# Optimization experiments

Measured on AMD Instinct MI355X. Metric: run time of the kernel, lower is better.

The kernel has to match this reference:

```python
import jax, jax.numpy as jnp
import numpy as np

N, S, D, H, NF, E = 65536, 24, 64, 4, 256, 1048576
Hd = D // H
EPS = 1e-5


def _pe_table(nf, d):
    pe = np.zeros((nf, d), np.float32)
    pos = np.arange(nf, dtype=np.float32)[:, None]
    div = np.exp(np.arange(0, d, 2, dtype=np.float32) * -(np.log(10000.0) / d))
    pe[:, 0::2] = np.sin(pos * div)
    pe[:, 1::2] = np.cos(pos * div)
    return jnp.asarray(pe)


def setup_inputs() -> dict:
    key = jax.random.key(0)
    ks = iter(jax.random.split(key, 64))
    g = lambda shape: jax.random.normal(next(ks), shape, jnp.float32) * 0.02
    z = lambda shape: jnp.zeros(shape, jnp.float32)
    o = lambda shape: jnp.ones(shape, jnp.float32)
    inp = {
        'x': jax.random.normal(next(ks), (N, S), jnp.float32),
        'edge_index': jax.random.randint(next(ks), (2, E), 0, N, jnp.int32),
        'Wi': g((S, D)), 'bi': z((D,)), 'pe': _pe_table(NF, D),
        # per-head TransformerConv params (H separate convs, heads=1 each)
        'Wq': g((H, D, Hd)), 'Wk': g((H, D, Hd)), 'Wv': g((H, D, Hd)),
        'bq': z((H, Hd)), 'bk': z((H, Hd)), 'bv': z((H, Hd)),
        'Ws': g((H, D, Hd)), 'bs': z((H, Hd)),
        'Wo': g((D, D)), 'bo': z((D,)), 'gln_g': o((D,)), 'gln_b': z((D,)),
        # temporal MHA + FFN
        'Wqt': g((D, D)), 'Wkt': g((D, D)), 'Wvt': g((D, D)),
        'bqt': z((D,)), 'bkt': z((D,)), 'bvt': z((D,)),
        'Wot': g((D, D)), 'bot': z((D,)),
        'ln1_g': o((D,)), 'ln1_b': z((D,)),
        'W1': g((D, 2 * D)), 'b1': z((2 * D,)), 'W2': g((2 * D, D)), 'b2': z((D,)),
        'ln2_g': o((D,)), 'ln2_b': z((D,)),
        # aggregation + prediction head
        'Wa1': g((NF * D, D)), 'ba1': z((D,)), 'Wa2': g((D, D // 2)), 'ba2': z((D // 2,)),
        'Wh1': g((D // 2, D // 4)), 'bh1': z((D // 4,)), 'Wh2': g((D // 4, 1)), 'bh2': z((1,)),
    }
    return inp


def _ln(x, g, b):
    m = jnp.mean(x, axis=-1, keepdims=True)
    v = jnp.var(x, axis=-1, keepdims=True)
    return (x - m) * jax.lax.rsqrt(v + EPS) * g + b


def reference(x, edge_index, Wi, bi, pe, Wq, Wk, Wv, bq, bk, bv, Ws, bs, Wo, bo,
              gln_g, gln_b, Wqt, Wkt, Wvt, bqt, bkt, bvt, Wot, bot, ln1_g, ln1_b,
              W1, b1, W2, b2, ln2_g, ln2_b, Wa1, ba1, Wa2, ba2, Wh1, bh1, Wh2, bh2):
    n, nf, d = x.shape[0], pe.shape[0], pe.shape[1]
    bsz = n // nf
    scale = 1.0 / np.sqrt(Hd).astype(np.float32)

    # input projection + positional encoding (repeated per graph)
    h = x @ Wi + bi + jnp.tile(pe, (bsz, 1))  # [N, D]

    # ---- multi-head TransformerConv graph attention (gather-softmax-scatter) ----
    src, dst = edge_index[0], edge_index[1]
    q = jnp.einsum('nd,hdk->nhk', h, Wq) + bq  # [N,H,Hd]
    k = jnp.einsum('nd,hdk->nhk', h, Wk) + bk
    v = jnp.einsum('nd,hdk->nhk', h, Wv) + bv
    logits = jnp.sum(q[dst] * k[src], axis=-1) * scale  # [E,H]
    m = jax.ops.segment_max(logits, dst, num_segments=N)  # [N,H]
    ex = jnp.exp(logits - m[dst])
    denom = jax.ops.segment_sum(ex, dst, num_segments=N)  # [N,H]
    alpha = ex / denom[dst]
    agg = jax.ops.segment_sum(alpha[:, :, None] * v[src], dst, num_segments=N)  # [N,H,Hd]
    skip = jnp.einsum('nd,hdk->nhk', h, Ws) + bs  # root weight (lin_skip)
    out = (agg + skip).reshape(n, d) @ Wo + bo
    h = _ln(out + h, gln_g, gln_b)  # residual (in_dim == out_dim)

    # ---- temporal transformer over the NF node axis ----
    xt = h.reshape(bsz, nf, d)
    qt = (xt @ Wqt + bqt).reshape(bsz, nf, H, Hd)
    kt = (xt @ Wkt + bkt).reshape(bsz, nf, H, Hd)
    vt = (xt @ Wvt + bvt).reshape(bsz, nf, H, Hd)
    sc = jnp.einsum('bihd,bjhd->bhij', qt, kt) * scale
    a = jax.nn.softmax(sc, axis=-1)
    attn = jnp.einsum('bhij,bjhd->bihd', a, vt).reshape(bsz, nf, d)
    attn = attn @ Wot + bot
    xt = _ln(xt + attn, ln1_g, ln1_b)
    ff = jax.nn.relu(xt @ W1 + b1) @ W2 + b2
    xt = _ln(xt + ff, ln2_g, ln2_b)

    # ---- aggregation + prediction head ----
    xf = xt.reshape(bsz, nf * d)
    a1 = jax.nn.relu(xf @ Wa1 + ba1)
    a2 = jax.nn.relu(a1 @ Wa2 + ba2)
    h1 = jax.nn.relu(a2 @ Wh1 + bh1)
    out = jax.nn.sigmoid(h1 @ Wh2 + bh2)
    return out.squeeze(-1)  # [B]
```

## Files before the change

kernel.cpp:

```cpp
#include <hip/hip_runtime.h>
#include <hip/hip_fp16.h>
#include <math.h>

#define NN 65536
#define SIN 24
#define DD 64
#define HH 4
#define HDIM 16
#define NFRM 256
#define NE 1048576
#define BSZ 256
#define EPSLN 1e-5f
#define SCL 0.25f
#define AKS 32
#define WTN 55296

typedef __attribute__((ext_vector_type(8))) short bf16x8;
typedef __attribute__((ext_vector_type(4))) float f32x4;

__device__ __forceinline__ unsigned short f2bf(float f) {
  unsigned u = __float_as_uint(f);
  return (unsigned short)((u + 0x7FFFu + ((u >> 16) & 1u)) >> 16);
}
__device__ __forceinline__ float bf2f(unsigned short b) {
  return __uint_as_float(((unsigned)b) << 16);
}
__device__ __forceinline__ float bflo(unsigned u) {
  return __uint_as_float(u << 16);
}
__device__ __forceinline__ float bfhi(unsigned u) {
  return __uint_as_float(u & 0xFFFF0000u);
}
__device__ __forceinline__ unsigned f2e5(float f) {
  unsigned short h = __half_as_ushort(__float2half(f));
  unsigned r = (unsigned)h + 0x7Fu + ((h >> 8) & 1u);
  return (r >> 8) & 0xFFu;
}
__device__ __forceinline__ float h2fb(unsigned short b) {
  return __half2float(__ushort_as_half(b));
}
#define KLO(u) h2fb((unsigned short)((u) & 0xFF00u))
#define KHI(u) h2fb((unsigned short)(((u) >> 16) & 0xFF00u))
#define VLO(u) h2fb((unsigned short)(((u) << 8) & 0xFF00u))
#define VHI(u) h2fb((unsigned short)(((u) >> 8) & 0xFF00u))

__device__ __forceinline__ void stage_bf(const unsigned short* __restrict__ src,
                                         unsigned short* dst, int n8, int DK, int ST, int tid) {
  int dk8 = DK >> 3;
  for (int idx = tid; idx < n8; idx += 256) {
    int row = idx / dk8, c = (idx % dk8) * 8;
    *(uint4*)(dst + row * ST + c) = *(const uint4*)(src + (size_t)row * DK + c);
  }
}

__global__ void k_wprep(const float* __restrict__ Wo, const float* __restrict__ Wot,
                        const float* __restrict__ Wqt, const float* __restrict__ Wkt,
                        const float* __restrict__ Wvt, const float* __restrict__ W1,
                        const float* __restrict__ W2, const float* __restrict__ Wq,
                        const float* __restrict__ Wk, const float* __restrict__ Wv,
                        const float* __restrict__ Wsk, const float* __restrict__ Wi,
                        unsigned short* __restrict__ wt) {
  int i = blockIdx.x * 256 + threadIdx.x;
  if (i >= WTN) return;
  float v;
  if (i < 4096)       { int t = i;         int j = t >> 6, d = t & 63; v = Wo[d * 64 + j]; }
  else if (i < 8192)  { int t = i - 4096;  int j = t >> 6, d = t & 63; v = Wot[d * 64 + j]; }
  else if (i < 12288) { int t = i - 8192;  int j = t >> 6, d = t & 63; v = Wqt[d * 64 + j]; }
  else if (i < 16384) { int t = i - 12288; int j = t >> 6, d = t & 63; v = Wkt[d * 64 + j]; }
  else if (i < 20480) { int t = i - 16384; int j = t >> 6, d = t & 63; v = Wvt[d * 64 + j]; }
  else if (i < 28672) { int t = i - 20480; int j = t >> 6, d = t & 63; v = W1[d * 128 + j]; }
  else if (i < 36864) { int t = i - 28672; int j = t >> 7, d = t & 127; v = W2[d * 64 + j]; }
  else if (i < 40960) { int t = i - 36864; int j = t >> 6, d = t & 63; v = Wq[(j >> 4) * 1024 + d * 16 + (j & 15)]; }
  else if (i < 45056) { int t = i - 40960; int j = t >> 6, d = t & 63; v = Wk[(j >> 4) * 1024 + d * 16 + (j & 15)]; }
  else if (i < 49152) { int t = i - 45056; int j = t >> 6, d = t & 63; v = Wv[(j >> 4) * 1024 + d * 16 + (j & 15)]; }
  else if (i < 53248) { int t = i - 49152; int j = t >> 6, d = t & 63; v = Wsk[(j >> 4) * 1024 + d * 16 + (j & 15)]; }
  else                { int t = i - 53248; int j = t >> 5, k = t & 31; v = (k < SIN) ? Wi[k * 64 + j] : 0.f; }
  wt[i] = f2bf(v);
}

__global__ void k_wprep2(const float* __restrict__ Wa1, unsigned short* __restrict__ wa1t) {
  __shared__ float tile[64][65];
  int kb = blockIdx.x;
  int t = threadIdx.x;
  int c = t & 63, r0 = t >> 6;
  int k0 = kb * 64;
#pragma unroll
  for (int i = 0; i < 16; ++i) {
    int r = r0 + i * 4;
    tile[r][c] = Wa1[(size_t)(k0 + r) * 64 + c];
  }
  __syncthreads();
#pragma unroll
  for (int i = 0; i < 16; ++i) {
    int o = r0 + i * 4;
    wa1t[(size_t)o * 16384 + k0 + c] = f2bf(tile[c][o]);
  }
}

__global__ void __launch_bounds__(256)
k_qkvs_m(const float* __restrict__ x, const unsigned short* __restrict__ wt,
         const float* __restrict__ bi, const float* __restrict__ pe,
         const float* __restrict__ bq, const float* __restrict__ bk,
         const float* __restrict__ bv, const float* __restrict__ bs,
         unsigned short* __restrict__ us_h, unsigned short* __restrict__ us_q,
         unsigned short* __restrict__ kv8, unsigned short* __restrict__ us_sk) {
  __shared__ unsigned short Xs[64 * 72];
  __shared__ unsigned short Ws4[4 * 64 * 72];
  unsigned short* Xi  = Ws4;
  unsigned short* WiS = Ws4 + 64 * 40;
  int tid = threadIdx.x;
  int n0 = blockIdx.x * 64;
  for (int idx = tid; idx < 2048; idx += 256) {
    int row = idx >> 5, k = idx & 31;
    Xi[row * 40 + k] = (k < SIN) ? f2bf(x[(size_t)(n0 + row) * SIN + k]) : 0;
    WiS[row * 40 + k] = wt[53248 + row * 32 + k];
  }
  __syncthreads();
  int lane = tid & 63, w = tid >> 6;
  int c = lane & 15, g = lane >> 4;
  int rowb = n0 + w * 16 + 4 * g;
  f32x4 hb[4];
  {
    bf16x8 xf = *(const bf16x8*)(Xi + (w * 16 + c) * 40 + g * 8);
#pragma unroll
    for (int jj = 0; jj < 4; ++jj)
      hb[jj] = __builtin_amdgcn_mfma_f32_16x16x32_bf16(xf,
                 *(const bf16x8*)(WiS + (jj * 16 + c) * 40 + g * 8),
                 (f32x4){0.f, 0.f, 0.f, 0.f}, 0, 0, 0);
  }
#pragma unroll
  for (int jj = 0; jj < 4; ++jj) {
    int col = jj * 16 + c;
    float bb = bi[col];
#pragma unroll
    for (int r = 0; r < 4; ++r) {
      int row = w * 16 + 4 * g + r;
      float hv = hb[jj][r] + bb + pe[((n0 + row) & (NFRM - 1)) * DD + col];
      unsigned short hbf = f2bf(hv);
      us_h[(size_t)(n0 + row) * DD + col] = hbf;
      Xs[row * 72 + col] = hbf;
    }
  }
  __syncthreads();
  stage_bf(wt + 36864, Ws4, 64 * 8, 64, 72, tid);
  stage_bf(wt + 40960, Ws4 + 4608, 64 * 8, 64, 72, tid);
  stage_bf(wt + 45056, Ws4 + 9216, 64 * 8, 64, 72, tid);
  stage_bf(wt + 49152, Ws4 + 13824, 64 * 8, 64, 72, tid);
  __syncthreads();
  f32x4 aq[4], ak[4], av[4], as_[4];
#pragma unroll
  for (int jj = 0; jj < 4; ++jj) {
#pragma unroll
    for (int r = 0; r < 4; ++r) { aq[jj][r] = 0.f; ak[jj][r] = 0.f; av[jj][r] = 0.f; as_[jj][r] = 0.f; }
  }
  const unsigned short* xrow = Xs + (w * 16 + c) * 72 + g * 8;
#pragma unroll
  for (int kk = 0; kk < 2; ++kk) {
    bf16x8 af = *(const bf16x8*)(xrow + kk * 32);
#pragma unroll
    for (int jj = 0; jj < 4; ++jj) {
      int boff = (jj * 16 + c) * 72 + kk * 32 + g * 8;
      aq[jj] = __builtin_amdgcn_mfma_f32_16x16x32_bf16(af, *(const bf16x8*)(Ws4 + boff), aq[jj], 0, 0, 0);
      ak[jj] = __builtin_amdgcn_mfma_f32_16x16x32_bf16(af, *(const bf16x8*)(Ws4 + 4608 + boff), ak[jj], 0, 0, 0);
      av[jj] = __builtin_amdgcn_mfma_f32_16x16x32_bf16(af, *(const bf16x8*)(Ws4 + 9216 + boff), av[jj], 0, 0, 0);
      as_[jj] = __builtin_amdgcn_mfma_f32_16x16x32_bf16(af, *(const bf16x8*)(Ws4 + 13824 + boff), as_[jj], 0, 0, 0);
    }
  }
#pragma unroll
  for (int jj = 0; jj < 4; ++jj) {
    int col = jj * 16 + c;
    float bqj = bq[col], bkj = bk[col], bvj = bv[col], bsj = bs[col];
#pragma unroll
    for (int r = 0; r < 4; ++r) {
      size_t o = (size_t)(rowb + r) * 64 + col;
      us_q[o] = f2bf(aq[jj][r] + bqj);
      kv8[o] = (unsigned short)((f2e5(ak[jj][r] + bkj) << 8) | f2e5(av[jj][r] + bvj));
      us_sk[o] = f2bf(as_[jj][r] + bsj);
    }
  }
}

__global__ void k_hist(const int* __restrict__ ei, int* __restrict__ hist) {
  __shared__ int h2[2][256];
  int t = threadIdx.x;
  h2[0][t] = 0; h2[1][t] = 0;
  __syncthreads();
  int sub = (t >> 6) & 1;
  int base = blockIdx.x * 4096;
#pragma unroll
  for (int r = 0; r < 16; ++r)
    atomicAdd(&h2[sub][ei[NE + base + r * 256 + t] >> 8], 1);
  __syncthreads();
  hist[t * 256 + blockIdx.x] = h2[0][t] + h2[1][t];
}

__global__ void k_hscan(int* __restrict__ hist, int* __restrict__ btot) {
  __shared__ int s[256];
  int t = threadIdx.x, bkt = blockIdx.x;
  int v = hist[bkt * 256 + t];
  s[t] = v; __syncthreads();
  for (int off = 1; off < 256; off <<= 1) {
    int x = (t >= off) ? s[t - off] : 0;
    __syncthreads();
    s[t] += x;
    __syncthreads();
  }
  hist[bkt * 256 + t] = s[t] - v;
  if (t == 255) btot[bkt] = s[255];
}

__global__ void k_bscan(const int* __restrict__ btot, int* __restrict__ bbase) {
  __shared__ int s[256];
  int t = threadIdx.x;
  int v = btot[t];
  s[t] = v; __syncthreads();
  for (int off = 1; off < 256; off <<= 1) {
    int x = (t >= off) ? s[t - off] : 0;
    __syncthreads();
    s[t] += x;
    __syncthreads();
  }
  bbase[t] = s[t] - v;
}

__global__ void k_passB(const int* __restrict__ ei, const int* __restrict__ hist,
                        const int* __restrict__ bbase, int* __restrict__ pairs) {
  __shared__ int cur[256];
  int t = threadIdx.x;
  cur[t] = bbase[t] + hist[t * 256 + blockIdx.x];
  __syncthreads();
  int base = blockIdx.x * 4096;
#pragma unroll
  for (int r = 0; r < 16; ++r) {
    int e = base + r * 256 + t;
    int src = ei[e], dst = ei[NE + e];
    int pos = atomicAdd(&cur[dst >> 8], 1);
    pairs[pos] = ((dst & 255) << 16) | src;
  }
}

__global__ void k_passC(const int* __restrict__ pairs, const int* __restrict__ bbase,
                        const int* __restrict__ btot, int* __restrict__ rowptr,
                        int* __restrict__ srcs) {
  __shared__ int cnt[256];
  __shared__ int s[256];
  int t = threadIdx.x, bkt = blockIdx.x;
  cnt[t] = 0;
  __syncthreads();
  int base = bbase[bkt], n = btot[bkt];
  int pr[18];
#pragma unroll
  for (int j = 0; j < 18; ++j) {
    int i = t + j * 256;
    if (i >= n) break;
    int p = pairs[base + i];
    pr[j] = p;
    atomicAdd(&cnt[p >> 16], 1);
  }
  for (int i = t + 18 * 256; i < n; i += 256)
    atomicAdd(&cnt[pairs[base + i] >> 16], 1);
  __syncthreads();
  int v = cnt[t];
  s[t] = v; __syncthreads();
  for (int off = 1; off < 256; off <<= 1) {
    int x = (t >= off) ? s[t - off] : 0;
    __syncthreads();
    s[t] += x;
    __syncthreads();
  }
  int rp = base + s[t] - v;
  rowptr[bkt * 256 + t] = rp;
  if (bkt == 0 && t == 0) rowptr[NN] = NE;
  __syncthreads();
  cnt[t] = rp;
  __syncthreads();
#pragma unroll
  for (int j = 0; j < 18; ++j) {
    int i = t + j * 256;
    if (i >= n) break;
    int p = pr[j];
    int pos = atomicAdd(&cnt[p >> 16], 1);
    srcs[pos] = p & 0xFFFF;
  }
  for (int i = t + 18 * 256; i < n; i += 256) {
    int p = pairs[base + i];
    int pos = atomicAdd(&cnt[p >> 16], 1);
    srcs[pos] = p & 0xFFFF;
  }
}

__global__ void __launch_bounds__(256)
k_gattn(const unsigned short* __restrict__ us_q, const unsigned short* __restrict__ kv8,
        const int* __restrict__ rowptr, const int* __restrict__ srcs,
        const unsigned short* __restrict__ us_sk, unsigned short* __restrict__ tmpb) {
  __shared__ float red[8][32][17];
  int tid = threadIdx.x;
  int lane = tid & 63;
  int slot = (tid >> 5) & 7;
  int e = (lane >> 2) & 7, h = lane & 3;
  int dst = (blockIdx.x << 3) + slot;
  float qv[16];
  {
    const uint4* qp = (const uint4*)(us_q + (size_t)dst * 64 + h * 16);
    uint4 q0 = qp[0], q1 = qp[1];
    qv[0] = bflo(q0.x); qv[1] = bfhi(q0.x); qv[2] = bflo(q0.y); qv[3] = bfhi(q0.y);
    qv[4] = bflo(q0.z); qv[5] = bfhi(q0.z); qv[6] = bflo(q0.w); qv[7] = bfhi(q0.w);
    qv[8] = bflo(q1.x); qv[9] = bfhi(q1.x); qv[10] = bflo(q1.y); qv[11] = bfhi(q1.y);
    qv[12] = bflo(q1.z); qv[13] = bfhi(q1.z); qv[14] = bflo(q1.w); qv[15] = bfhi(q1.w);
  }
  int beg = rowptr[dst], end = rowptr[dst + 1];
  float l = 0.f;
  float acc[16];
#pragma unroll
  for (int i = 0; i < 16; ++i) acc[i] = 0.f;

  int idx = beg + e;
  int src = (idx < end) ? srcs[idx] : 0;
  const uint4* kp = (const uint4*)(kv8 + (size_t)src * 64 + h * 16);
  uint4 A = kp[0], Bv = kp[1];
  for (;;) {
    int nidx = idx + 8;
    bool any_next = __any(nidx < end);
    uint4 nA, nB;
    if (any_next) {
      int nsrc = (nidx < end) ? srcs[nidx] : 0;
      const uint4* np = (const uint4*)(kv8 + (size_t)nsrc * 64 + h * 16);
      nA = np[0]; nB = np[1];
    }
    bool valid = idx < end;
    float s;
    s  = KLO(A.x) * qv[0]   + KHI(A.x) * qv[1]   + KLO(A.y) * qv[2]   + KHI(A.y) * qv[3];
    s += KLO(A.z) * qv[4]   + KHI(A.z) * qv[5]   + KLO(A.w) * qv[6]   + KHI(A.w) * qv[7];
    s += KLO(Bv.x) * qv[8]  + KHI(Bv.x) * qv[9]  + KLO(Bv.y) * qv[10] + KHI(Bv.y) * qv[11];
    s += KLO(Bv.z) * qv[12] + KHI(Bv.z) * qv[13] + KLO(Bv.w) * qv[14] + KHI(Bv.w) * qv[15];
    float pex = valid ? __expf(s * SCL) : 0.f;
    l += pex;
    acc[0]  += pex * VLO(A.x);  acc[1]  += pex * VHI(A.x);
    acc[2]  += pex * VLO(A.y);  acc[3]  += pex * VHI(A.y);
    acc[4]  += pex * VLO(A.z);  acc[5]  += pex * VHI(A.z);
    acc[6]  += pex * VLO(A.w);  acc[7]  += pex * VHI(A.w);
    acc[8]  += pex * VLO(Bv.x); acc[9]  += pex * VHI(Bv.x);
    acc[10] += pex * VLO(Bv.y); acc[11] += pex * VHI(Bv.y);
    acc[12] += pex * VLO(Bv.z); acc[13] += pex * VHI(Bv.z);
    acc[14] += pex * VLO(Bv.w); acc[15] += pex * VHI(Bv.w);
    if (!any_next) break;
    A = nA; Bv = nB;
    idx = nidx;
  }
  l += __shfl_xor(l, 4); l += __shfl_xor(l, 8); l += __shfl_xor(l, 16);
  float* rw = &red[slot][lane & 31][0];
#pragma unroll
  for (int i = 0; i < 16; ++i) rw[i] = acc[i];
  int r32 = lane & 31;
  int h0 = r32 >> 4, i0 = r32 & 15;
  float l0 = __shfl(l, (lane & 32) + h0);
  float l1 = __shfl(l, (lane & 32) + h0 + 2);
  float s0 = 0.f, s1 = 0.f;
#pragma unroll
  for (int ep = 0; ep < 8; ++ep) {
    s0 += red[slot][ep * 4 + h0][i0];
    s1 += red[slot][ep * 4 + h0 + 2][i0];
  }
  bool nonempty = end > beg;
  float a0 = nonempty ? s0 / l0 : 0.f;
  float a1 = nonempty ? s1 / l1 : 0.f;
  size_t o0 = (size_t)dst * 64 + r32;
  tmpb[o0] = f2bf(a0 + bf2f(us_sk[o0]));
  tmpb[o0 + 32] = f2bf(a1 + bf2f(us_sk[o0 + 32]));
}

__global__ void __launch_bounds__(256)
k_mlqkvt(const unsigned short* __restrict__ in1, const unsigned short* __restrict__ wt,
         const float* __restrict__ bias, const float* __restrict__ gam,
         const float* __restrict__ bet, unsigned short* __restrict__ us_h,
         const float* __restrict__ bqt, const float* __restrict__ bkt,
         const float* __restrict__ bvt,
         unsigned short* __restrict__ qt, unsigned short* __restrict__ kt,
         unsigned short* __restrict__ vt) {
  __shared__ unsigned short A[64 * 72];
  __shared__ unsigned short B[3 * 64 * 72];
  int tid = threadIdx.x;
  int n0 = blockIdx.x * 64;
  stage_bf(in1 + (size_t)n0 * 64, A, 64 * 8, 64, 72, tid);
  stage_bf(wt + 0, B, 64 * 8, 64, 72, tid);
  __syncthreads();
  int lane = tid & 63, w = tid >> 6;
  int c = lane & 15, g = lane >> 4;
  f32x4 acc[4];
#pragma unroll
  for (int j = 0; j < 4; ++j) { acc[j][0] = 0.f; acc[j][1] = 0.f; acc[j][2] = 0.f; acc[j][3] = 0.f; }
  const unsigned short* xrow = A + (w * 16 + c) * 72 + g * 8;
#pragma unroll
  for (int kk = 0; kk < 2; ++kk) {
    bf16x8 af = *(const bf16x8*)(xrow + kk * 32);
#pragma unroll
    for (int j = 0; j < 4; ++j)
      acc[j] = __builtin_amdgcn_mfma_f32_16x16x32_bf16(af,
                 *(const bf16x8*)(B + (j * 16 + c) * 72 + kk * 32 + g * 8), acc[j], 0, 0, 0);
  }
  int rowb = n0 + w * 16 + 4 * g;
  float o[4][4];
#pragma unroll
  for (int j = 0; j < 4; ++j) {
    int col = j * 16 + c;
    float bb = bias[col];
#pragma unroll
    for (int r = 0; r < 4; ++r)
      o[j][r] = acc[j][r] + bb + bf2f(us_h[(size_t)(rowb + r) * 64 + col]);
  }
#pragma unroll
  for (int r = 0; r < 4; ++r) {
    float s = (o[0][r] + o[1][r]) + (o[2][r] + o[3][r]);
    float s2 = (o[0][r] * o[0][r] + o[1][r] * o[1][r]) + (o[2][r] * o[2][r] + o[3][r] * o[3][r]);
#pragma unroll
    for (int off = 1; off <= 8; off <<= 1) {
      s += __shfl_xor(s, off);
      s2 += __shfl_xor(s2, off);
    }
    float mean = s * (1.0f / 64.0f);
    float var = s2 * (1.0f / 64.0f) - mean * mean;
    float rs = rsqrtf(var + EPSLN);
#pragma unroll
    for (int j = 0; j < 4; ++j)
      o[j][r] = (o[j][r] - mean) * rs * gam[j * 16 + c] + bet[j * 16 + c];
  }
  __syncthreads();
#pragma unroll
  for (int j = 0; j < 4; ++j) {
    int col = j * 16 + c;
#pragma unroll
    for (int r = 0; r < 4; ++r) {
      unsigned short ob = f2bf(o[j][r]);
      us_h[(size_t)(rowb + r) * 64 + col] = ob;
      A[(w * 16 + 4 * g + r) * 72 + col] = ob;
    }
  }
  stage_bf(wt + 8192, B, 64 * 8, 64, 72, tid);
  stage_bf(wt + 12288, B + 4608, 64 * 8, 64, 72, tid);
  stage_bf(wt + 16384, B + 9216, 64 * 8, 64, 72, tid);
  __syncthreads();
  f32x4 aq[4], ak[4], av[4];
#pragma unroll
  for (int j = 0; j < 4; ++j) {
#pragma unroll
    for (int r = 0; r < 4; ++r) { aq[j][r] = 0.f; ak[j][r] = 0.f; av[j][r] = 0.f; }
  }
#pragma unroll
  for (int kk = 0; kk < 2; ++kk) {
    bf16x8 af = *(const bf16x8*)(xrow + kk * 32);
#pragma unroll
    for (int j = 0; j < 4; ++j) {
      int boff = (j * 16 + c) * 72 + kk * 32 + g * 8;
      aq[j] = __builtin_amdgcn_mfma_f32_16x16x32_bf16(af, *(const bf16x8*)(B + boff), aq[j], 0, 0, 0);
      ak[j] = __builtin_amdgcn_mfma_f32_16x16x32_bf16(af, *(const bf16x8*)(B + 4608 + boff), ak[j], 0, 0, 0);
      av[j] = __builtin_amdgcn_mfma_f32_16x16x32_bf16(af, *(const bf16x8*)(B + 9216 + boff), av[j], 0, 0, 0);
    }
  }
#pragma unroll
  for (int j = 0; j < 4; ++j) {
    int col = j * 16 + c;
    float bqj = bqt[col], bkj = bkt[col], bvj = bvt[col];
#pragma unroll
    for (int r = 0; r < 4; ++r) {
      size_t oo = (size_t)j * (NN * 16) + (size_t)(rowb + r) * 16 + c;
      qt[oo] = f2bf(aq[j][r] + bqj);
      kt[oo] = f2bf(ak[j][r] + bkj);
      vt[oo] = f2bf(av[j][r] + bvj);
    }
  }
}

#define PST 40
#define VTS 264
__global__ void __launch_bounds__(256)
k_tattn(const unsigned short* __restrict__ qtb, const unsigned short* __restrict__ ktb,
        const unsigned short* __restrict__ vtb, unsigned short* __restrict__ attnb) {
  int b = blockIdx.x >> 2, hh = blockIdx.x & 3;
  __shared__ unsigned short Qs[NFRM][16];
  __shared__ unsigned short Ks[NFRM][16];
  __shared__ unsigned short Vt[16][VTS];
  __shared__ unsigned short Ps[4][16][PST];
  int t = threadIdx.x;
  int wv = t >> 6, lane = t & 63;
  int g = lane >> 4, c = lane & 15;
  {
    size_t src = (size_t)hh * (NN * 16) + ((size_t)b * NFRM + t) * 16;
    const uint4* qsrc = (const uint4*)(qtb + src);
    const uint4* ksrc = (const uint4*)(ktb + src);
    const uint4* vsrc = (const uint4*)(vtb + src);
    ((uint4*)Qs[t])[0] = qsrc[0]; ((uint4*)Qs[t])[1] = qsrc[1];
    ((uint4*)Ks[t])[0] = ksrc[0]; ((uint4*)Ks[t])[1] = ksrc[1];
    uint4 v0 = vsrc[0], v1 = vsrc[1];
    unsigned vv[8] = {v0.x, v0.y, v0.z, v0.w, v1.x, v1.y, v1.z, v1.w};
#pragma unroll
    for (int d = 0; d < 8; ++d) {
      Vt[2 * d][t] = (unsigned short)(vv[d] & 0xFFFFu);
      Vt[2 * d + 1][t] = (unsigned short)(vv[d] >> 16);
    }
  }
  __syncthreads();
  const bf16x8 zf = {0, 0, 0, 0, 0, 0, 0, 0};
  unsigned short (*P)[PST] = Ps[wv];
  for (int qt0 = wv; qt0 < 16; qt0 += 4) {
    bf16x8 qf = zf;
    if (g < 2) qf = *(const bf16x8*)&Qs[qt0 * 16 + c][g * 8];
    f32x4 O = {0.f, 0.f, 0.f, 0.f};
    float lacc[4] = {0.f, 0.f, 0.f, 0.f};
    for (int jp = 0; jp < 8; ++jp) {
#pragma unroll
      for (int half = 0; half < 2; ++half) {
        int jt = jp * 2 + half;
        bf16x8 kf = zf;
        if (g < 2) kf = *(const bf16x8*)&Ks[jt * 16 + c][g * 8];
        f32x4 S = __builtin_amdgcn_mfma_f32_16x16x32_bf16(qf, kf,
                    (f32x4){0.f, 0.f, 0.f, 0.f}, 0, 0, 0);
#pragma unroll
        for (int r = 0; r < 4; ++r) {
          float p = __expf(S[r] * SCL);
          lacc[r] += p;
          P[4 * g + r][half * 16 + c] = f2bf(p);
        }
      }
      bf16x8 pf = *(const bf16x8*)&P[c][g * 8];
      bf16x8 vf = *(const bf16x8*)&Vt[c][jp * 32 + g * 8];
      O = __builtin_amdgcn_mfma_f32_16x16x32_bf16(pf, vf, O, 0, 0, 0);
    }
#pragma unroll
    for (int r = 0; r < 4; ++r) {
      float s = lacc[r];
      s += __shfl_xor(s, 1); s += __shfl_xor(s, 2);
      s += __shfl_xor(s, 4); s += __shfl_xor(s, 8);
      lacc[r] = 1.0f / s;
    }
    size_t obase = ((size_t)b * NFRM + qt0 * 16) * DD + hh * 16;
#pragma unroll
    for (int r = 0; r < 4; ++r)
      attnb[obase + (size_t)(4 * g + r) * DD + c] = f2bf(O[r] * lacc[r]);
  }
}

__global__ void __launch_bounds__(256)
k_blk2(const unsigned short* __restrict__ attn, const unsigned short* __restrict__ wt,
       const unsigned short* __restrict__ res, const float* __restrict__ bot,
       const float* __restrict__ l1g, const float* __restrict__ l1b,
       const float* __restrict__ b1, const float* __restrict__ b2,
       const float* __restrict__ l2g, const float* __restrict__ l2b,
       unsigned short* __restrict__ xtb) {
  __shared__ unsigned short XLs[64 * 72];
  __shared__ unsigned short BufW[128 * 72];
  __shared__ unsigned short BufX[64 * 136];
  int tid = threadIdx.x;
  int n0 = blockIdx.x * 64;
  int lane = tid & 63, w = tid >> 6;
  int c = lane & 15, g = lane >> 4;
  int rowb = n0 + w * 16 + 4 * g;
  stage_bf(attn + (size_t)n0 * 64, BufX, 64 * 8, 64, 72, tid);
  stage_bf(wt + 4096, BufW, 64 * 8, 64, 72, tid);
  __syncthreads();
  f32x4 acc[4];
#pragma unroll
  for (int j = 0; j < 4; ++j) { acc[j][0] = 0.f; acc[j][1] = 0.f; acc[j][2] = 0.f; acc[j][3] = 0.f; }
  const unsigned short* xrow = BufX + (w * 16 + c) * 72 + g * 8;
#pragma unroll
  for (int kk = 0; kk < 2; ++kk) {
    bf16x8 af = *(const bf16x8*)(xrow + kk * 32);
#pragma unroll
    for (int j = 0; j < 4; ++j)
      acc[j] = __builtin_amdgcn_mfma_f32_16x16x32_bf16(af,
                 *(const bf16x8*)(BufW + (j * 16 + c) * 72 + kk * 32 + g * 8), acc[j], 0, 0, 0);
  }
  float x[4][4];
#pragma unroll
  for (int j = 0; j < 4; ++j) {
    int col = j * 16 + c;
    float bb = bot[col];
#pragma unroll
    for (int r = 0; r < 4; ++r)
      x[j][r] = acc[j][r] + bb + bf2f(res[(size_t)(rowb + r) * 64 + col]);
  }
#pragma unroll
  for (int r = 0; r < 4; ++r) {
    float s = (x[0][r] + x[1][r]) + (x[2][r] + x[3][r]);
    float s2 = (x[0][r] * x[0][r] + x[1][r] * x[1][r]) + (x[2][r] * x[2][r] + x[3][r] * x[3][r]);
#pragma unroll
    for (int off = 1; off <= 8; off <<= 1) {
      s += __shfl_xor(s, off);
      s2 += __shfl_xor(s2, off);
    }
    float mean = s * (1.0f / 64.0f);
    float var = s2 * (1.0f / 64.0f) - mean * mean;
    float rs = rsqrtf(var + EPSLN);
#pragma unroll
    for (int j = 0; j < 4; ++j)
      x[j][r] = (x[j][r] - mean) * rs * l1g[j * 16 + c] + l1b[j * 16 + c];
  }
  __syncthreads();
#pragma unroll
  for (int j = 0; j < 4; ++j)
#pragma unroll
    for (int r = 0; r < 4; ++r)
      XLs[(w * 16 + 4 * g + r) * 72 + j * 16 + c] = f2bf(x[j][r]);
  stage_bf(wt + 20480, BufW, 128 * 8, 64, 72, tid);
  __syncthreads();
  f32x4 ua[8];
#pragma unroll
  for (int j = 0; j < 8; ++j) { ua[j][0] = 0.f; ua[j][1] = 0.f; ua[j][2] = 0.f; ua[j][3] = 0.f; }
  const unsigned short* xrow2 = XLs + (w * 16 + c) * 72 + g * 8;
#pragma unroll
  for (int kk = 0; kk < 2; ++kk) {
    bf16x8 af = *(const bf16x8*)(xrow2 + kk * 32);
#pragma unroll
    for (int j = 0; j < 8; ++j)
      ua[j] = __builtin_amdgcn_mfma_f32_16x16x32_bf16(af,
                *(const bf16x8*)(BufW + (j * 16 + c) * 72 + kk * 32 + g * 8), ua[j], 0, 0, 0);
  }
#pragma unroll
  for (int j = 0; j < 8; ++j) {
    int col = j * 16 + c;
    float bb = b1[col];
#pragma unroll
    for (int r = 0; r < 4; ++r)
      BufX[(w * 16 + 4 * g + r) * 136 + col] = f2bf(fmaxf(ua[j][r] + bb, 0.f));
  }
  __syncthreads();
  stage_bf(wt + 28672, BufW, 64 * 16, 128, 136, tid);
  __syncthreads();
  f32x4 ya[4];
#pragma unroll
  for (int j = 0; j < 4; ++j) { ya[j][0] = 0.f; ya[j][1] = 0.f; ya[j][2] = 0.f; ya[j][3] = 0.f; }
  const unsigned short* urow = BufX + (w * 16 + c) * 136 + g * 8;
#pragma unroll
  for (int kk = 0; kk < 4; ++kk) {
    bf16x8 af = *(const bf16x8*)(urow + kk * 32);
#pragma unroll
    for (int j = 0; j < 4; ++j)
      ya[j] = __builtin_amdgcn_mfma_f32_16x16x32_bf16(af,
                *(const bf16x8*)(BufW + (j * 16 + c) * 136 + kk * 32 + g * 8), ya[j], 0, 0, 0);
  }
  float o2[4][4];
#pragma unroll
  for (int j = 0; j < 4; ++j) {
    int col = j * 16 + c;
    float bb = b2[col];
#pragma unroll
    for (int r = 0; r < 4; ++r)
      o2[j][r] = ya[j][r] + bb + x[j][r];
  }
#pragma unroll
  for (int r = 0; r < 4; ++r) {
    float s = (o2[0][r] + o2[1][r]) + (o2[2][r] + o2[3][r]);
    float s2 = (o2[0][r] * o2[0][r] + o2[1][r] * o2[1][r]) + (o2[2][r] * o2[2][r] + o2[3][r] * o2[3][r]);
#pragma unroll
    for (int off = 1; off <= 8; off <<= 1) {
      s += __shfl_xor(s, off);
      s2 += __shfl_xor(s2, off);
    }
    float mean = s * (1.0f / 64.0f);
    float var = s2 * (1.0f / 64.0f) - mean * mean;
    float rs = rsqrtf(var + EPSLN);
#pragma unroll
    for (int j = 0; j < 4; ++j)
      xtb[(size_t)(rowb + r) * 64 + j * 16 + c] =
          f2bf((o2[j][r] - mean) * rs * l2g[j * 16 + c] + l2b[j * 16 + c]);
  }
}

__global__ void __launch_bounds__(256)
k_agg1a_m(const unsigned short* __restrict__ xtb, const unsigned short* __restrict__ wa1t,
          float* __restrict__ part) {
  int ks = blockIdx.x >> 2, mt = blockIdx.x & 3;
  int t = threadIdx.x, lane = t & 63, w = t >> 6;
  int c = lane & 15, g = lane >> 4;
  int m0 = mt * 64;
  int k0 = ks * 512;
  f32x4 acc[4];
#pragma unroll
  for (int j = 0; j < 4; ++j) { acc[j][0] = 0.f; acc[j][1] = 0.f; acc[j][2] = 0.f; acc[j][3] = 0.f; }
  const unsigned short* arow = xtb + (size_t)(m0 + w * 16 + c) * 16384 + k0 + g * 8;
  const unsigned short* brow = wa1t + (size_t)c * 16384 + k0 + g * 8;
#pragma unroll 4
  for (int kk = 0; kk < 16; ++kk) {
    bf16x8 af = *(const bf16x8*)(arow + kk * 32);
#pragma unroll
    for (int j = 0; j < 4; ++j)
      acc[j] = __builtin_amdgcn_mfma_f32_16x16x32_bf16(af,
                 *(const bf16x8*)(brow + (size_t)j * 16 * 16384 + kk * 32), acc[j], 0, 0, 0);
  }
  int rowb = m0 + w * 16 + 4 * g;
#pragma unroll
  for (int j = 0; j < 4; ++j)
#pragma unroll
    for (int r = 0; r < 4; ++r)
      part[(size_t)ks * (BSZ * DD) + (size_t)(rowb + r) * 64 + j * 16 + c] = acc[j][r];
}

__global__ void k_head(const float* __restrict__ part, const float* __restrict__ ba1,
                       const float* __restrict__ Wa2, const float* __restrict__ ba2,
                       const float* __restrict__ Wh1, const float* __restrict__ bh1,
                       const float* __restrict__ Wh2, const float* __restrict__ bh2,
                       float* __restrict__ out) {
  int b = blockIdx.x, t = threadIdx.x;
  __shared__ float s1[64], s2[32], s3[16];
  float a0 = ba1[t];
#pragma unroll 8
  for (int ks = 0; ks < AKS; ++ks) a0 += part[(size_t)ks * (BSZ * DD) + b * 64 + t];
  s1[t] = fmaxf(a0, 0.f);
  __syncthreads();
  if (t < 32) {
    float a = ba2[t];
#pragma unroll 8
    for (int j = 0; j < 64; ++j) a += s1[j] * Wa2[j * 32 + t];
    s2[t] = fmaxf(a, 0.f);
  }
  __syncthreads();
  if (t < 16) {
    float a = bh1[t];
#pragma unroll
    for (int j = 0; j < 32; ++j) a += s2[j] * Wh1[j * 16 + t];
    s3[t] = fmaxf(a, 0.f);
  }
  __syncthreads();
  if (t == 0) {
    float a = bh2[0];
#pragma unroll
    for (int j = 0; j < 16; ++j) a += s3[j] * Wh2[j];
    out[b] = 1.0f / (1.0f + expf(-a));
  }
}

extern "C" void kernel_launch(void* const* d_in, const int* in_sizes, int n_in,
                              void* d_out, int out_size, void* d_ws, size_t ws_size,
                              hipStream_t stream) {
  const float* x   = (const float*)d_in[0];
  const int*   ei  = (const int*)d_in[1];
  const float* Wi  = (const float*)d_in[2];
  const float* bi  = (const float*)d_in[3];
  const float* pe  = (const float*)d_in[4];
  const float* Wq  = (const float*)d_in[5];
  const float* Wk  = (const float*)d_in[6];
  const float* Wv  = (const float*)d_in[7];
  const float* bq  = (const float*)d_in[8];
  const float* bk  = (const float*)d_in[9];
  const float* bv  = (const float*)d_in[10];
  const float* Ws  = (const float*)d_in[11];
  const float* bs  = (const float*)d_in[12];
  const float* Wo  = (const float*)d_in[13];
  const float* bo  = (const float*)d_in[14];
  const float* gg  = (const float*)d_in[15];
  const float* gb  = (const float*)d_in[16];
  const float* Wqt = (const float*)d_in[17];
  const float* Wkt = (const float*)d_in[18];
  const float* Wvt = (const float*)d_in[19];
  const float* bqt = (const float*)d_in[20];
  const float* bkt = (const float*)d_in[21];
  const float* bvt = (const float*)d_in[22];
  const float* Wot = (const float*)d_in[23];
  const float* bot = (const float*)d_in[24];
  const float* l1g = (const float*)d_in[25];
  const float* l1b = (const float*)d_in[26];
  const float* W1  = (const float*)d_in[27];
  const float* b1  = (const float*)d_in[28];
  const float* W2  = (const float*)d_in[29];
  const float* b2  = (const float*)d_in[30];
  const float* l2g = (const float*)d_in[31];
  const float* l2b = (const float*)d_in[32];
  const float* Wa1 = (const float*)d_in[33];
  const float* ba1 = (const float*)d_in[34];
  const float* Wa2 = (const float*)d_in[35];
  const float* ba2 = (const float*)d_in[36];
  const float* Wh1 = (const float*)d_in[37];
  const float* bh1 = (const float*)d_in[38];
  const float* Wh2 = (const float*)d_in[39];
  const float* bh2 = (const float*)d_in[40];
  float* out = (float*)d_out;

  const size_t ND = (size_t)NN * DD;

  unsigned short* us_h  = (unsigned short*)d_ws;
  unsigned short* us_q  = us_h + ND;
  unsigned short* kv8   = us_q + ND;
  unsigned short* us_sk = kv8 + ND;
  unsigned short* tmpb  = us_sk + ND;
  unsigned short* us_qt = tmpb + ND;
  unsigned short* us_kt = us_qt + ND;
  unsigned short* us_vt = us_kt + ND;
  unsigned short* attnb = us_vt + ND;
  unsigned short* xtb   = attnb + ND;
  float* f_part = (float*)(xtb + ND);
  int* i_srcs   = (int*)(f_part + (size_t)AKS * BSZ * DD);
  int* i_rowptr = i_srcs + NE;
  int* i_hist   = i_rowptr + NN + 4;
  int* i_btot   = i_hist + 65536;
  int* i_bbase  = i_btot + 256;
  int* i_pairs  = i_bbase + 256;
  unsigned short* wt = (unsigned short*)(i_pairs + NE);
  unsigned short* wa1t = wt + WTN;

  dim3 B(256);
  k_wprep<<<dim3((WTN + 255) / 256), B, 0, stream>>>(Wo, Wot, Wqt, Wkt, Wvt, W1, W2,
                                                     Wq, Wk, Wv, Ws, Wi, wt);
  k_wprep2<<<dim3(256), B, 0, stream>>>(Wa1, wa1t);
  k_qkvs_m<<<dim3(NN / 64), B, 0, stream>>>(x, wt, bi, pe, bq, bk, bv, bs,
                                            us_h, us_q, kv8, us_sk);
  k_hist <<<dim3(256), B, 0, stream>>>(ei, i_hist);
  k_hscan<<<dim3(256), B, 0, stream>>>(i_hist, i_btot);
  k_bscan<<<dim3(1),   B, 0, stream>>>(i_btot, i_bbase);
  k_passB<<<dim3(256), B, 0, stream>>>(ei, i_hist, i_bbase, i_pairs);
  k_passC<<<dim3(256), B, 0, stream>>>(i_pairs, i_bbase, i_btot, i_rowptr, i_srcs);
  k_gattn<<<dim3(NN / 8), B, 0, stream>>>(us_q, kv8, i_rowptr, i_srcs, us_sk, tmpb);
  k_mlqkvt<<<dim3(NN / 64), B, 0, stream>>>(tmpb, wt, bo, gg, gb, us_h,
                                            bqt, bkt, bvt, us_qt, us_kt, us_vt);
  k_tattn<<<dim3(BSZ * HH), B, 0, stream>>>(us_qt, us_kt, us_vt, attnb);
  k_blk2<<<dim3(NN / 64), B, 0, stream>>>(attnb, wt, us_h, bot, l1g, l1b, b1, b2,
                                          l2g, l2b, xtb);
  k_agg1a_m<<<dim3(AKS * 4), B, 0, stream>>>(xtb, wa1t, f_part);
  k_head<<<dim3(BSZ), dim3(64), 0, stream>>>(f_part, ba1, Wa2, ba2, Wh1, bh1, Wh2, bh2, out);
}
```

Before: 170.8 us.

## Fold bucket scan into passB/passC, use 16-bit source indices, prefetch srcs

Removes the single-block k_bscan launch by recomputing the 256-entry bucket prefix scan redundantly inside every block of passB and passC. Source indices are stored as unsigned short instead of int, halving the CSR srcs traffic. The graph-attention loop preloads the first three source indices up front to shorten the dependent index-then-gather chain. The cost is redundant scan work in each block and extra registers in k_gattn.

```diff
diff --git a/kernel.cpp b/kernel.cpp
--- a/kernel.cpp
+++ b/kernel.cpp
@@ -209,25 +209,20 @@
   if (t == 255) btot[bkt] = s[255];
 }
 
-__global__ void k_bscan(const int* __restrict__ btot, int* __restrict__ bbase) {
-  __shared__ int s[256];
+__global__ void k_passB(const int* __restrict__ ei, const int* __restrict__ hist,
+                        const int* __restrict__ btot, int* __restrict__ pairs) {
+  __shared__ int cur[256];
+  __shared__ int sc[256];
   int t = threadIdx.x;
   int v = btot[t];
-  s[t] = v; __syncthreads();
+  sc[t] = v; __syncthreads();
   for (int off = 1; off < 256; off <<= 1) {
-    int x = (t >= off) ? s[t - off] : 0;
+    int x = (t >= off) ? sc[t - off] : 0;
     __syncthreads();
-    s[t] += x;
+    sc[t] += x;
     __syncthreads();
   }
-  bbase[t] = s[t] - v;
-}
-
-__global__ void k_passB(const int* __restrict__ ei, const int* __restrict__ hist,
-                        const int* __restrict__ bbase, int* __restrict__ pairs) {
-  __shared__ int cur[256];
-  int t = threadIdx.x;
-  cur[t] = bbase[t] + hist[t * 256 + blockIdx.x];
+  cur[t] = (sc[t] - v) + hist[t * 256 + blockIdx.x];
   __syncthreads();
   int base = blockIdx.x * 4096;
 #pragma unroll
@@ -239,15 +234,26 @@
   }
 }
 
-__global__ void k_passC(const int* __restrict__ pairs, const int* __restrict__ bbase,
-                        const int* __restrict__ btot, int* __restrict__ rowptr,
-                        int* __restrict__ srcs) {
+__global__ void k_passC(const int* __restrict__ pairs, const int* __restrict__ btot,
+                        int* __restrict__ rowptr, unsigned short* __restrict__ srcs) {
   __shared__ int cnt[256];
   __shared__ int s[256];
+  __shared__ int eb[256];
   int t = threadIdx.x, bkt = blockIdx.x;
+  {
+    int v0 = btot[t];
+    s[t] = v0; __syncthreads();
+    for (int off = 1; off < 256; off <<= 1) {
+      int x = (t >= off) ? s[t - off] : 0;
+      __syncthreads();
+      s[t] += x;
+      __syncthreads();
+    }
+    eb[t] = s[t] - v0;
+  }
   cnt[t] = 0;
   __syncthreads();
-  int base = bbase[bkt], n = btot[bkt];
+  int base = eb[bkt], n = btot[bkt];
   int pr[18];
 #pragma unroll
   for (int j = 0; j < 18; ++j) {
@@ -280,18 +286,18 @@
     if (i >= n) break;
     int p = pr[j];
     int pos = atomicAdd(&cnt[p >> 16], 1);
-    srcs[pos] = p & 0xFFFF;
+    srcs[pos] = (unsigned short)(p & 0xFFFF);
   }
   for (int i = t + 18 * 256; i < n; i += 256) {
     int p = pairs[base + i];
     int pos = atomicAdd(&cnt[p >> 16], 1);
-    srcs[pos] = p & 0xFFFF;
+    srcs[pos] = (unsigned short)(p & 0xFFFF);
   }
 }
 
 __global__ void __launch_bounds__(256)
 k_gattn(const unsigned short* __restrict__ us_q, const unsigned short* __restrict__ kv8,
-        const int* __restrict__ rowptr, const int* __restrict__ srcs,
+        const int* __restrict__ rowptr, const unsigned short* __restrict__ srcs,
         const unsigned short* __restrict__ us_sk, unsigned short* __restrict__ tmpb) {
   __shared__ float red[8][32][17];
   int tid = threadIdx.x;
@@ -315,15 +321,20 @@
   for (int i = 0; i < 16; ++i) acc[i] = 0.f;
 
   int idx = beg + e;
-  int src = (idx < end) ? srcs[idx] : 0;
-  const uint4* kp = (const uint4*)(kv8 + (size_t)src * 64 + h * 16);
+  int src0 = (idx < end) ? (int)srcs[idx] : 0;
+  int psrc1 = (idx + 8 < end) ? (int)srcs[idx + 8] : 0;
+  int psrc2 = (idx + 16 < end) ? (int)srcs[idx + 16] : 0;
+  const uint4* kp = (const uint4*)(kv8 + (size_t)src0 * 64 + h * 16);
   uint4 A = kp[0], Bv = kp[1];
+  int batch = 0;
   for (;;) {
     int nidx = idx + 8;
     bool any_next = __any(nidx < end);
     uint4 nA, nB;
     if (any_next) {
-      int nsrc = (nidx < end) ? srcs[nidx] : 0;
+      int nsrc = (batch == 0) ? psrc1
+               : (batch == 1) ? psrc2
+               : ((nidx < end) ? (int)srcs[nidx] : 0);
       const uint4* np = (const uint4*)(kv8 + (size_t)nsrc * 64 + h * 16);
       nA = np[0]; nB = np[1];
     }
@@ -346,6 +357,7 @@
     if (!any_next) break;
     A = nA; Bv = nB;
     idx = nidx;
+    ++batch;
   }
   l += __shfl_xor(l, 4); l += __shfl_xor(l, 8); l += __shfl_xor(l, 16);
   float* rw = &red[slot][lane & 31][0];
@@ -787,12 +799,11 @@
   unsigned short* attnb = us_vt + ND;
   unsigned short* xtb   = attnb + ND;
   float* f_part = (float*)(xtb + ND);
-  int* i_srcs   = (int*)(f_part + (size_t)AKS * BSZ * DD);
-  int* i_rowptr = i_srcs + NE;
+  unsigned short* us_srcs = (unsigned short*)(f_part + (size_t)AKS * BSZ * DD);
+  int* i_rowptr = (int*)(us_srcs + NE);
   int* i_hist   = i_rowptr + NN + 4;
   int* i_btot   = i_hist + 65536;
-  int* i_bbase  = i_btot + 256;
-  int* i_pairs  = i_bbase + 256;
+  int* i_pairs  = i_btot + 256;
   unsigned short* wt = (unsigned short*)(i_pairs + NE);
   unsigned short* wa1t = wt + WTN;
 
@@ -804,10 +815,9 @@
                                             us_h, us_q, kv8, us_sk);
   k_hist <<<dim3(256), B, 0, stream>>>(ei, i_hist);
   k_hscan<<<dim3(256), B, 0, stream>>>(i_hist, i_btot);
-  k_bscan<<<dim3(1),   B, 0, stream>>>(i_btot, i_bbase);
-  k_passB<<<dim3(256), B, 0, stream>>>(ei, i_hist, i_bbase, i_pairs);
-  k_passC<<<dim3(256), B, 0, stream>>>(i_pairs, i_bbase, i_btot, i_rowptr, i_srcs);
-  k_gattn<<<dim3(NN / 8), B, 0, stream>>>(us_q, kv8, i_rowptr, i_srcs, us_sk, tmpb);
+  k_passB<<<dim3(256), B, 0, stream>>>(ei, i_hist, i_btot, i_pairs);
+  k_passC<<<dim3(256), B, 0, stream>>>(i_pairs, i_btot, i_rowptr, us_srcs);
+  k_gattn<<<dim3(NN / 8), B, 0, stream>>>(us_q, kv8, i_rowptr, us_srcs, us_sk, tmpb);
   k_mlqkvt<<<dim3(NN / 64), B, 0, stream>>>(tmpb, wt, bo, gg, gb, us_h,
                                             bqt, bkt, bvt, us_qt, us_kt, us_vt);
   k_tattn<<<dim3(BSZ * HH), B, 0, stream>>>(us_qt, us_kt, us_vt, attnb);
```

New measurement: 167.8 us. No clear change (-1.8%).
